# Kernel tuning notes

Hardware: AMD Instinct MI355X
Metric: run time of the kernel (lower is better)

Reference implementation:

```python
import jax, jax.numpy as jnp
import numpy as np

EPS = 1e-6
NMS_THR = 0.5
PULL_W = 1.0
PUSH_W = 1.0


def bbox_overlaps(a, b):
    # a: [M,4], b: [N,4] in (x1,y1,x2,y2) -> IoU [M,N]
    area_a = (a[:, 2] - a[:, 0]) * (a[:, 3] - a[:, 1])
    area_b = (b[:, 2] - b[:, 0]) * (b[:, 3] - b[:, 1])
    lt = jnp.maximum(a[:, None, :2], b[None, :, :2])
    rb = jnp.minimum(a[:, None, 2:], b[None, :, 2:])
    wh = jnp.clip(rb - lt, 0.0)
    inter = wh[..., 0] * wh[..., 1]
    return inter / (area_a[:, None] + area_b[None, :] - inter + EPS)


def _single_nms_loss(gti, gt_box, proposals):
    # gti: [N] int, gt_box: [G,4], proposals: [N,5]
    N = proposals.shape[0]
    G = gt_box.shape[0]
    boxes = proposals[:, :4]
    scores = proposals[:, 4]
    # push_select=True: first arg of proposal-proposal IoU is detached
    iou = bbox_overlaps(jax.lax.stop_gradient(boxes), boxes)      # [N,N]
    gpi = bbox_overlaps(gt_box, boxes)                            # [G,N]
    gpi_per = gpi[gti, jnp.arange(N)]                             # gt_proposal_iou[gt_inds[s], s]
    sg_scores = jax.lax.stop_gradient(scores)

    pos = gti >= 0
    n_pos = jnp.sum(pos)
    zero = jnp.zeros((), proposals.dtype)
    rec0 = jnp.full((G,), -1, jnp.int32)   # max_score_box_rec: gt -> box idx

    def step(carry, _):
        active, rec, pull_sum, push_sum, pull_cnt, push_cnt = carry
        any_act = jnp.any(active)
        i = jnp.argmax(jnp.where(active, scores, -jnp.inf))
        i_gt = gti[i]
        rem = active.at[i].set(False)
        has_rem = jnp.any(rem)
        body_valid = any_act & has_rem  # torch breaks before adding losses if idx empty

        # ----- pull -----
        seen = rec[i_gt] >= 0
        max_idx = jnp.maximum(rec[i_gt], 0)
        max_s_iou = jnp.maximum(iou[max_idx, i], EPS)
        pull = -jnp.log(1.0 - NMS_THR + max_s_iou) * sg_scores[i]
        pull_sum = pull_sum + jnp.where(any_act & seen & has_rem, pull, 0.0)
        pull_cnt = pull_cnt + jnp.where(any_act & seen, 1.0, 0.0)  # incremented before break
        new_val = jnp.where(any_act & ~seen, i.astype(rec.dtype), rec[i_gt])
        rec = rec.at[i_gt].set(new_val)

        # ----- push -----
        overlap = rem & (iou[i] > NMS_THR)
        push_mask = overlap & (gti != i_gt)
        has_push = jnp.any(push_mask)
        seen_s = rec[gti] >= 0  # rec already contains i_gt here (matches torch order)
        q = push_mask & (~seen_s)
        cnt = jnp.sum(q.astype(scores.dtype)) + EPS
        per = -jnp.log(EPS + gpi_per) * sg_scores
        push = jnp.sum(jnp.where(q, per, 0.0)) / cnt
        push_sum = push_sum + jnp.where(body_valid & has_push, push, 0.0)
        push_cnt = push_cnt + jnp.where(body_valid & has_push, 1.0, 0.0)

        active_next = rem & (~overlap)
        return (active_next, rec, pull_sum, push_sum, pull_cnt, push_cnt), None

    init = (pos, rec0, zero, zero, zero, zero)
    (_, _, pull_sum, push_sum, pull_cnt, push_cnt), _ = jax.lax.scan(step, init, None, length=N)

    gate = (n_pos > 1).astype(proposals.dtype)  # early-return when <=1 positive
    pull = gate * pull_sum / (pull_cnt + EPS)
    push = gate * push_sum / (push_cnt + EPS)
    return push, pull


def setup_inputs() -> dict:
    key = jax.random.key(0)
    k0, k1, k2, k3, k4, k5, k6 = jax.random.split(key, 7)
    B, N, G = 8, 2048, 64
    anchor_gt_inds = jax.random.randint(k0, (B, N), 0, G)
    # valid GT boxes: centers in a 1000x1000 image, sizes in [16,128]
    cx = jax.random.uniform(k1, (B, G)) * 1000.0
    cy = jax.random.uniform(k2, (B, G)) * 1000.0
    w = 16.0 + jax.random.uniform(k3, (B, G)) * 112.0
    h = 16.0 + jax.random.uniform(k4, (B, G)) * 112.0
    gt_bboxes = jnp.stack([cx - w / 2, cy - h / 2, cx + w / 2, cy + h / 2], axis=-1).astype(jnp.float32)
    # proposals jitter around their assigned GT so pull/push branches trigger
    pb = gt_bboxes[jnp.arange(B)[:, None], anchor_gt_inds] + jax.random.normal(k5, (B, N, 4)) * 6.0
    x1 = jnp.minimum(pb[..., 0], pb[..., 2]); x2 = jnp.maximum(pb[..., 0], pb[..., 2]) + 1.0
    y1 = jnp.minimum(pb[..., 1], pb[..., 3]); y2 = jnp.maximum(pb[..., 1], pb[..., 3]) + 1.0
    scores = jax.random.uniform(k6, (B, N))
    proposal_list = jnp.stack([x1, y1, x2, y2, scores], axis=-1).astype(jnp.float32)
    return {"gt_inds": anchor_gt_inds, "anchor_gt_inds": anchor_gt_inds,
            "gt_bboxes": gt_bboxes, "proposal_list": proposal_list}


def reference(gt_inds, anchor_gt_inds, gt_bboxes, proposal_list):
    # gt_inds is overwritten by anchor_gt_inds in the original code
    push, pull = jax.vmap(_single_nms_loss)(anchor_gt_inds, gt_bboxes, proposal_list)
    return jnp.stack([jnp.mean(push) * PUSH_W, jnp.mean(pull) * PULL_W])
```

## Files before the change

kernel.cpp:

```cpp
#include <hip/hip_runtime.h>
#include <math.h>
#include <limits.h>

#define EPSF 1e-6f
#define THR 0.5f
#define PUSH_W 1.0f
#define PULL_W 1.0f

constexpr int BN = 2048;
constexpr int BG = 64;

__device__ __forceinline__ float iou_box(float4 a, float4 b) {
  float aa = (a.z - a.x) * (a.w - a.y);
  float ab = (b.z - b.x) * (b.w - b.y);
  float w = fmaxf(fminf(a.z, b.z) - fmaxf(a.x, b.x), 0.f);
  float h = fmaxf(fminf(a.w, b.w) - fmaxf(a.y, b.y), 0.f);
  float inter = w * h;
  return inter / (aa + ab - inter + EPSF);
}

__global__ __launch_bounds__(512) void k1_sort(
    const int* __restrict__ gti_all, const float* __restrict__ gtb_all,
    const float* __restrict__ prop_all,
    float4* __restrict__ boxs, float* __restrict__ pers,
    short* __restrict__ gtss, float* __restrict__ scs,
    int* __restrict__ arrive)
{
  const int b = blockIdx.x & 7;
  const int sub = blockIdx.x >> 3;
  const int tid = threadIdx.x;
  __shared__ unsigned long long key[BN];

  if (blockIdx.x == 0 && tid == 0) *arrive = 0;

  const float* P = prop_all + (size_t)b * BN * 5;
  const int* gti = gti_all + b * BN;
  const float* GB = gtb_all + b * BG * 4;

  for (int k = 0; k < 4; ++k) {
    int j = tid + k * 512;
    key[j] = ((unsigned long long)__float_as_uint(P[j * 5 + 4]) << 32) |
             (unsigned)(BN - 1 - j);
  }
  __syncthreads();

  const int r = sub * 64 + (tid >> 3);
  const int g8 = tid & 7;
  const unsigned long long myk = key[r];
  int cnt = 0;
  const ulonglong2* K2 = (const ulonglong2*)key;
#pragma unroll 8
  for (int i = 0; i < 128; ++i) {
    ulonglong2 kk = K2[g8 + 8 * i];
    cnt += (kk.x > myk) ? 1 : 0;
    cnt += (kk.y > myk) ? 1 : 0;
  }
  cnt += __shfl_down(cnt, 4, 8);
  cnt += __shfl_down(cnt, 2, 8);
  cnt += __shfl_down(cnt, 1, 8);
  if (g8 == 0) {
    const int rank = cnt;
    int idx = (BN - 1) - (int)(myk & 0xffffffffu);
    float x1 = P[idx * 5 + 0], y1 = P[idx * 5 + 1];
    float x2 = P[idx * 5 + 2], y2 = P[idx * 5 + 3];
    float s = __uint_as_float((unsigned)(myk >> 32));
    int g = gti[idx];
    float4 bx = make_float4(x1, y1, x2, y2);
    boxs[b * BN + rank] = bx;
    scs[b * BN + rank] = s;
    gtss[b * BN + rank] = (short)g;
    float pv = 0.f;
    if (g >= 0) {
      float4 gb = make_float4(GB[g * 4], GB[g * 4 + 1], GB[g * 4 + 2], GB[g * 4 + 3]);
      pv = -logf(EPSF + iou_box(gb, bx)) * s;
    }
    pers[b * BN + rank] = pv;
  }
}

__global__ __launch_bounds__(512) void k2_adj(
    const float4* __restrict__ boxs, uint2* __restrict__ adjC)
{
  const int b  = blockIdx.x & 7;
  const int rg = (blockIdx.x >> 3) & 7;
  const int cg = blockIdx.x >> 6;
  const int tid = threadIdx.x;
  const int lane = tid & 63;
  const int w = tid >> 6;
  __shared__ float4 bs[512];

  const float4* B = boxs + b * BN;
  bs[tid] = B[cg * 512 + tid];

  const float4 r0 = B[rg * 256 +   0 + lane];
  const float4 r1 = B[rg * 256 +  64 + lane];
  const float4 r2 = B[rg * 256 + 128 + lane];
  const float4 r3 = B[rg * 256 + 192 + lane];
  const float a0 = (r0.z - r0.x) * (r0.w - r0.y) + EPSF;
  const float a1 = (r1.z - r1.x) * (r1.w - r1.y) + EPSF;
  const float a2 = (r2.z - r2.x) * (r2.w - r2.y) + EPSF;
  const float a3 = (r3.z - r3.x) * (r3.w - r3.y) + EPSF;
  __syncthreads();

  const float4* C = &bs[w * 64];
  unsigned lo0 = 0, lo1 = 0, lo2 = 0, lo3 = 0;
  unsigned hi0 = 0, hi1 = 0, hi2 = 0, hi3 = 0;

#define PRED(RR, AA, BJ, AB)                                              \
  (3.0f * (fmaxf(fminf(RR.z, BJ.z) - fmaxf(RR.x, BJ.x), 0.f) *            \
           fmaxf(fminf(RR.w, BJ.w) - fmaxf(RR.y, BJ.y), 0.f)) > AA + AB)

#pragma unroll 8
  for (int jj = 0; jj < 32; ++jj) {
    float4 bj = C[jj];
    float ab = (bj.z - bj.x) * (bj.w - bj.y);
    lo0 |= PRED(r0, a0, bj, ab) ? (1u << jj) : 0u;
    lo1 |= PRED(r1, a1, bj, ab) ? (1u << jj) : 0u;
    lo2 |= PRED(r2, a2, bj, ab) ? (1u << jj) : 0u;
    lo3 |= PRED(r3, a3, bj, ab) ? (1u << jj) : 0u;
  }
#pragma unroll 8
  for (int jj = 0; jj < 32; ++jj) {
    float4 bj = C[32 + jj];
    float ab = (bj.z - bj.x) * (bj.w - bj.y);
    hi0 |= PRED(r0, a0, bj, ab) ? (1u << jj) : 0u;
    hi1 |= PRED(r1, a1, bj, ab) ? (1u << jj) : 0u;
    hi2 |= PRED(r2, a2, bj, ab) ? (1u << jj) : 0u;
    hi3 |= PRED(r3, a3, bj, ab) ? (1u << jj) : 0u;
  }
#undef PRED

  const int c = cg * 8 + w;
  uint2* CO = adjC + ((size_t)b * 32 + c) * 2048;
  CO[rg * 256 +   0 + lane] = make_uint2(lo0, hi0);
  CO[rg * 256 +  64 + lane] = make_uint2(lo1, hi1);
  CO[rg * 256 + 128 + lane] = make_uint2(lo2, hi2);
  CO[rg * 256 + 192 + lane] = make_uint2(lo3, hi3);
}

#define QR(B, K, Q) B##_##K##_##Q

#define DECL16(B) \
  uint2 QR(B,0,0), QR(B,0,1), QR(B,0,2), QR(B,0,3), \
        QR(B,1,0), QR(B,1,1), QR(B,1,2), QR(B,1,3), \
        QR(B,2,0), QR(B,2,1), QR(B,2,2), QR(B,2,3), \
        QR(B,3,0), QR(B,3,1), QR(B,3,2), QR(B,3,3);

#define LOADCH(B, K, C) \
  QR(B,K,0) = Cb[(size_t)(C) * 2048 + wbase]; \
  QR(B,K,1) = Cb[(size_t)(C) * 2048 + wbase + 64]; \
  QR(B,K,2) = Cb[(size_t)(C) * 2048 + wbase + 128]; \
  QR(B,K,3) = Cb[(size_t)(C) * 2048 + wbase + 192];

#define LOAD16(B, RR) \
  LOADCH(B, 0, (RR)*4+0) LOADCH(B, 1, (RR)*4+1) \
  LOADCH(B, 2, (RR)*4+2) LOADCH(B, 3, (RR)*4+3)

#define PICK(B, K, C)                                                          \
  {                                                                            \
    unsigned mybit = ((act >> (K)) & ~(supG >> (K))) & 1u;                     \
    unsigned long long cand = __ballot(mybit != 0u);                           \
    unsigned long long pickw = 0ull;                                           \
    while (cand) {                                                             \
      int bpos = (int)__ffsll(cand) - 1;                                       \
      pickw |= 1ull << bpos;                                                   \
      unsigned rlo = __builtin_amdgcn_readlane(QR(B,K,K).x, bpos);             \
      unsigned rhi = __builtin_amdgcn_readlane(QR(B,K,K).y, bpos);             \
      cand &= ~((((unsigned long long)rhi) << 32) | (unsigned long long)rlo);  \
      cand &= ~(1ull << bpos);                                                 \
    }                                                                          \
    if (lane == 0) {                                                           \
      pm_lds[2 * (C)] = (unsigned)pickw;                                       \
      pm_lds[2 * (C) + 1] = (unsigned)(pickw >> 32);                           \
    }                                                                          \
    if (pickw != 0ull) {                                                       \
      unsigned pwlo = (unsigned)pickw, pwhi = (unsigned)(pickw >> 32);         \
      { unsigned hit = (QR(B,K,0).x & pwlo) | (QR(B,K,0).y & pwhi); supG |= (hit ? 1u : 0u); }      \
      { unsigned hit = (QR(B,K,1).x & pwlo) | (QR(B,K,1).y & pwhi); supG |= (hit ? 2u : 0u); }      \
      { unsigned hit = (QR(B,K,2).x & pwlo) | (QR(B,K,2).y & pwhi); supG |= (hit ? 4u : 0u); }      \
      { unsigned hit = (QR(B,K,3).x & pwlo) | (QR(B,K,3).y & pwhi); supG |= (hit ? 8u : 0u); }      \
    }                                                                          \
  }

#define APPLY(B, K, C)                                                         \
  {                                                                            \
    unsigned pwlo = pm_lds[2 * (C)], pwhi = pm_lds[2 * (C) + 1];               \
    if ((pwlo | pwhi) != 0u) {                                                 \
      unsigned nbits = 0;                                                      \
      { unsigned hit = (QR(B,K,0).x & pwlo) | (QR(B,K,0).y & pwhi); nbits |= hit ? 1u : 0u; }       \
      { unsigned hit = (QR(B,K,1).x & pwlo) | (QR(B,K,1).y & pwhi); nbits |= hit ? 2u : 0u; }       \
      { unsigned hit = (QR(B,K,2).x & pwlo) | (QR(B,K,2).y & pwhi); nbits |= hit ? 4u : 0u; }       \
      { unsigned hit = (QR(B,K,3).x & pwlo) | (QR(B,K,3).y & pwhi); nbits |= hit ? 8u : 0u; }       \
      unsigned flips = nbits & ~sup;                                           \
      sup |= nbits;                                                            \
      while (flips) {                                                          \
        int fq = __ffs(flips) - 1; flips &= flips - 1;                         \
        fsc_s[wbase + fq * 64] = (unsigned char)(C);                           \
      }                                                                        \
    }                                                                          \
  }

#define ROUND(RR, CUR, NXT)                                                    \
  {                                                                            \
    if (((RR) + 1 < 8) && (wave > (RR))) { LOAD16(NXT, (RR) + 1) }             \
    if (wave == (RR)) {                                                        \
      unsigned supG = sup;                                                     \
      PICK(CUR, 0, (RR)*4 + 0)                                                 \
      PICK(CUR, 1, (RR)*4 + 1)                                                 \
      PICK(CUR, 2, (RR)*4 + 2)                                                 \
      PICK(CUR, 3, (RR)*4 + 3)                                                 \
      asm volatile("s_waitcnt lgkmcnt(0)" ::: "memory");                       \
    }                                                                          \
    __builtin_amdgcn_s_barrier();                                              \
    asm volatile("" ::: "memory");                                             \
    if (wave >= (RR)) {                                                        \
      APPLY(CUR, 0, (RR)*4 + 0)                                                \
      APPLY(CUR, 1, (RR)*4 + 1)                                                \
      APPLY(CUR, 2, (RR)*4 + 2)                                                \
      APPLY(CUR, 3, (RR)*4 + 3)                                                \
    }                                                                          \
  }

__global__ __launch_bounds__(512, 1) void k3_fused(
    const float4* __restrict__ boxs, const float* __restrict__ pers,
    const short* __restrict__ gtss, const float* __restrict__ scs,
    const uint2* __restrict__ adjC, float* __restrict__ bp,
    int* __restrict__ arrive, float* __restrict__ out, int nb)
{
  const int b = blockIdx.x;
  const int tid = threadIdx.x;
  const int lane = tid & 63;
  const int wave = tid >> 6;

  __shared__ float qs_s[BN];
  __shared__ int qc_s[BN];
  __shared__ unsigned short ev_s[BN];
  __shared__ short gts_s[BN];
  __shared__ unsigned char fsc_s[BN];
  __shared__ unsigned pm_lds[64];
  __shared__ unsigned pre_s[64];
  __shared__ int fpr_s[64];
  __shared__ unsigned hp_s[64];
  __shared__ int lastrem_s, npick_s, npos_s;
  __shared__ float redp[8][4];

  const uint2* Cb = adjC + (size_t)b * 32 * 2048;
  const int wbase = wave * 256 + lane;

  for (int k = tid; k < BN / 2; k += 512)
    ((int*)gts_s)[k] = ((const int*)(gtss + b * BN))[k];
  for (int k = tid; k < BN; k += 512) { qs_s[k] = 0.f; qc_s[k] = 0; }
  for (int k = tid; k < BN; k += 512) fsc_s[k] = 255;
  if (tid < 64) { fpr_s[tid] = INT_MAX; hp_s[tid] = 0u; }
  if (tid == 0) { lastrem_s = 0; npos_s = 0; }
  __syncthreads();

  DECL16(X)
  DECL16(Y)
  LOAD16(X, 0)

  unsigned act = 0;
  if (gts_s[wbase +   0] >= 0) act |= 1u;
  if (gts_s[wbase +  64] >= 0) act |= 2u;
  if (gts_s[wbase + 128] >= 0) act |= 4u;
  if (gts_s[wbase + 192] >= 0) act |= 8u;
  {
    int cnt = __popc(act);
    for (int o = 1; o < 64; o <<= 1) cnt += __shfl_xor(cnt, o);
    if (lane == 0) atomicAdd(&npos_s, cnt);
  }
  unsigned sup = 0;

  ROUND(0, X, Y) ROUND(1, Y, X) ROUND(2, X, Y) ROUND(3, Y, X)
  ROUND(4, X, Y) ROUND(5, Y, X) ROUND(6, X, Y) ROUND(7, Y, X)

  __syncthreads();

  if (tid < 64) {
    int v = __popc(pm_lds[tid]);
    int inc = v;
    for (int o = 1; o < 64; o <<= 1) {
      int t = __shfl_up(inc, o);
      if (lane >= o) inc += t;
    }
    pre_s[tid] = (unsigned)(inc - v);
    if (tid == 63) npick_s = inc;
  }
  __syncthreads();
  if (wave == 0) {
    unsigned wbits = pm_lds[lane];
    int e = (int)pre_s[lane];
    while (wbits) {
      int bpos = __ffs(wbits) - 1; wbits &= wbits - 1;
      int rank = lane * 32 + bpos;
      ev_s[e] = (unsigned short)rank;
      atomicMin(&fpr_s[(int)gts_s[rank]], rank);
      e++;
    }
  }
  __syncthreads();

  const int P = npick_s;
  {
    const int j0 = tid, j1 = tid + 512, j2 = tid + 1024, j3 = tid + 1536;
    const int c0 = fsc_s[j0], c1 = fsc_s[j1], c2 = fsc_s[j2], c3 = fsc_s[j3];
    uint2 v0 = make_uint2(0, 0), v1 = v0, v2 = v0, v3 = v0;
    if (c0 != 255) v0 = Cb[(size_t)c0 * 2048 + j0];
    if (c1 != 255) v1 = Cb[(size_t)c1 * 2048 + j1];
    if (c2 != 255) v2 = Cb[(size_t)c2 * 2048 + j2];
    if (c3 != 255) v3 = Cb[(size_t)c3 * 2048 + j3];

#define PROCD(J, C, V)                                                         \
  {                                                                            \
    int gj = (int)gts_s[J];                                                    \
    if ((C) != 255 && gj >= 0) {                                               \
      unsigned m0 = V.x & pm_lds[2 * (C)];                                     \
      unsigned m1 = V.y & pm_lds[2 * (C) + 1];                                 \
      int frank = m0 ? ((C) * 64 + __ffs(m0) - 1)                              \
                     : ((C) * 64 + 32 + __ffs(m1) - 1);                        \
      if (frank != (J)) {                                                      \
        int e = (int)pre_s[frank >> 5] +                                       \
                __popc(pm_lds[frank >> 5] & ((1u << (frank & 31)) - 1u));      \
        if (e == P - 1) lastrem_s = 1;                                         \
        int gt = (int)gts_s[frank];                                            \
        if (gj != gt) {                                                        \
          atomicOr(&hp_s[e >> 5], 1u << (e & 31));                             \
          if (fpr_s[gj] > frank) {                                             \
            atomicAdd(&qs_s[e], pers[b * BN + (J)]);                           \
            atomicAdd(&qc_s[e], 1);                                            \
          }                                                                    \
        }                                                                      \
      }                                                                        \
    }                                                                          \
  }

    PROCD(j0, c0, v0)
    PROCD(j1, c1, v1)
    PROCD(j2, c2, v2)
    PROCD(j3, c3, v3)
#undef PROCD
  }
  __syncthreads();

  const int lastrem = lastrem_s;
  const int npos = npos_s;
  float pull_l = 0.f, pcl = 0.f, push_l = 0.f, pshl = 0.f;
  for (int t = tid; t < P; t += 512) {
    int r = (int)ev_s[t];
    int g = (int)gts_s[r];
    int fp = fpr_s[g];
    bool seen = (fp < r);
    bool hr = (t < P - 1) || (lastrem != 0);
    if (seen) {
      pcl += 1.f;
      if (hr) {
        float4 bA = boxs[b * BN + fp];
        float4 bB = boxs[b * BN + r];
        float io = iou_box(bA, bB);
        pull_l += -logf(1.f - THR + fmaxf(io, EPSF)) * scs[b * BN + r];
      }
    }
    if (hr && ((hp_s[t >> 5] >> (t & 31)) & 1u)) {
      pshl += 1.f;
      push_l += qs_s[t] / ((float)qc_s[t] + EPSF);
    }
  }
  for (int o = 1; o < 64; o <<= 1) {
    pull_l += __shfl_xor(pull_l, o);
    pcl    += __shfl_xor(pcl, o);
    push_l += __shfl_xor(push_l, o);
    pshl   += __shfl_xor(pshl, o);
  }
  if (lane == 0) { redp[wave][0] = pull_l; redp[wave][1] = pcl; redp[wave][2] = push_l; redp[wave][3] = pshl; }
  __syncthreads();
  if (tid == 0) {
    float Ps = 0.f, Pc = 0.f, Ss = 0.f, Sc = 0.f;
    for (int w = 0; w < 8; ++w) { Ps += redp[w][0]; Pc += redp[w][1]; Ss += redp[w][2]; Sc += redp[w][3]; }
    float gate = (npos > 1) ? 1.f : 0.f;
    bp[b * 2 + 0] = gate * Ss / (Sc + EPSF);
    bp[b * 2 + 1] = gate * Ps / (Pc + EPSF);
    __threadfence();
    int old = atomicAdd(arrive, 1);
    if (old == nb - 1) {
      __threadfence();
      float ps = 0.f, pl = 0.f;
      for (int i = 0; i < nb; ++i) { ps += bp[2 * i]; pl += bp[2 * i + 1]; }
      float inv = 1.f / (float)nb;
      out[0] = ps * inv * PUSH_W;
      out[1] = pl * inv * PULL_W;
      *arrive = 0;
    }
  }
}

constexpr int NT = 256;
constexpr int PT = BN / NT;
constexpr int NW = NT / 64;

__global__ void nms_finalize_kernel(const float* __restrict__ bp, float* __restrict__ out, int nb) {
  if (threadIdx.x == 0 && blockIdx.x == 0) {
    float ps = 0.f, pl = 0.f;
    for (int b = 0; b < nb; ++b) { ps += bp[2 * b]; pl += bp[2 * b + 1]; }
    float inv = 1.f / (float)nb;
    out[0] = ps * inv * PUSH_W;
    out[1] = pl * inv * PULL_W;
  }
}

__global__ __launch_bounds__(NT) void nms_loss_kernel(
    const int* __restrict__ gti_all, const float* __restrict__ gtb_all,
    const float* __restrict__ prop_all, float* __restrict__ out_bp)
{
  const int b = blockIdx.x;
  const int tid = threadIdx.x;
  const int lane = tid & 63;
  const int wave = tid >> 6;

  __shared__ float4 box[BN];
  __shared__ float sc[BN];
  __shared__ float per[BN];
  __shared__ int gts[BN];
  __shared__ unsigned char act[BN];
  __shared__ int rec[BG];
  __shared__ float rs[NW];
  __shared__ int ri[NW];
  __shared__ int rrem[NW];
  __shared__ int rqc[NW];
  __shared__ float rqs[NW];
  __shared__ int rany[NW];
  __shared__ int sh_nact;
  __shared__ int sh_ig;
  __shared__ float4 sh_ibox;

  const int* gti = gti_all + b * BN;
  const float* GB = gtb_all + b * BG * 4;
  const float* P = prop_all + (size_t)b * BN * 5;

  int local_pos = 0;
  for (int k = 0; k < PT; ++k) {
    int j = tid + k * NT;
    float x1 = P[j * 5 + 0], y1 = P[j * 5 + 1];
    float x2 = P[j * 5 + 2], y2 = P[j * 5 + 3];
    float s = P[j * 5 + 4];
    box[j] = make_float4(x1, y1, x2, y2);
    sc[j] = s;
    int g = gti[j];
    gts[j] = g;
    unsigned char a = (g >= 0) ? 1 : 0;
    act[j] = a;
    local_pos += a;
    float pv = 0.f;
    if (g >= 0) {
      float4 gb = make_float4(GB[g * 4], GB[g * 4 + 1], GB[g * 4 + 2], GB[g * 4 + 3]);
      float i2 = iou_box(gb, make_float4(x1, y1, x2, y2));
      pv = -logf(EPSF + i2) * s;
    }
    per[j] = pv;
  }
  if (tid < BG) rec[tid] = -1;
  for (int off = 32; off; off >>= 1) local_pos += __shfl_down(local_pos, off);
  if (lane == 0) rrem[wave] = local_pos;
  __syncthreads();
  int n_pos = 0;
  if (tid == 0) {
    for (int w = 0; w < NW; ++w) n_pos += rrem[w];
    sh_nact = n_pos;
  }
  float pull_sum = 0.f, push_sum = 0.f, pull_cnt = 0.f, push_cnt = 0.f;
  int t0_hasrem = 0;
  __syncthreads();

  while (true) {
    int nact = sh_nact;
    if (nact <= 0) break;
    float bs = -INFINITY;
    int bi = BN;
    for (int k = 0; k < PT; ++k) {
      int j = tid + k * NT;
      if (act[j]) {
        float s = sc[j];
        if (s > bs || (s == bs && j < bi)) { bs = s; bi = j; }
      }
    }
    for (int off = 32; off; off >>= 1) {
      float os = __shfl_down(bs, off);
      int oi = __shfl_down(bi, off);
      if (os > bs || (os == bs && oi < bi)) { bs = os; bi = oi; }
    }
    if (lane == 0) { rs[wave] = bs; ri[wave] = bi; }
    __syncthreads();
    if (tid == 0) {
      float cs = rs[0]; int ci = ri[0];
      for (int w = 1; w < NW; ++w)
        if (rs[w] > cs || (rs[w] == cs && ri[w] < ci)) { cs = rs[w]; ci = ri[w]; }
      int i = ci;
      int ig = gts[i];
      act[i] = 0;
      t0_hasrem = (nact - 1 > 0);
      int r = rec[ig];
      if (r >= 0) {
        pull_cnt += 1.f;
        if (t0_hasrem) {
          float i2 = iou_box(box[r], box[i]);
          float m = fmaxf(i2, EPSF);
          pull_sum += -logf(1.f - THR + m) * sc[i];
        }
      } else {
        rec[ig] = i;
      }
      sh_ig = ig; sh_ibox = box[i];
    }
    __syncthreads();
    float4 ib = sh_ibox;
    int igx = sh_ig;
    int removed = 0, qcc = 0, anyp = 0;
    float qss = 0.f;
    for (int k = 0; k < PT; ++k) {
      int j = tid + k * NT;
      if (act[j]) {
        float i2 = iou_box(ib, box[j]);
        if (i2 > THR) {
          act[j] = 0;
          removed++;
          int gj = gts[j];
          if (gj != igx) {
            anyp = 1;
            if (rec[gj] < 0) { qcc++; qss += per[j]; }
          }
        }
      }
    }
    for (int off = 32; off; off >>= 1) {
      removed += __shfl_down(removed, off);
      qcc += __shfl_down(qcc, off);
      qss += __shfl_down(qss, off);
      anyp |= __shfl_down(anyp, off);
    }
    if (lane == 0) { rrem[wave] = removed; rqc[wave] = qcc; rqs[wave] = qss; rany[wave] = anyp; }
    __syncthreads();
    if (tid == 0) {
      int rm = 0, qct = 0, ap = 0; float qst = 0.f;
      for (int w = 0; w < NW; ++w) { rm += rrem[w]; qct += rqc[w]; qst += rqs[w]; ap |= rany[w]; }
      sh_nact = nact - 1 - rm;
      if (t0_hasrem && ap) {
        push_sum += qst / ((float)qct + EPSF);
        push_cnt += 1.f;
      }
    }
    __syncthreads();
  }

  if (tid == 0) {
    float gate = (n_pos > 1) ? 1.f : 0.f;
    out_bp[b * 2 + 0] = gate * push_sum / (push_cnt + EPSF);
    out_bp[b * 2 + 1] = gate * pull_sum / (pull_cnt + EPSF);
  }
}

extern "C" void kernel_launch(void* const* d_in, const int* in_sizes, int n_in,
                              void* d_out, int out_size, void* d_ws, size_t ws_size,
                              hipStream_t stream) {
  const int* gti = (const int*)d_in[1];
  const float* gtb = (const float*)d_in[2];
  const float* props = (const float*)d_in[3];
  float* out = (float*)d_out;
  const int nb = in_sizes[1] / BN;

  const size_t off_adj  = 0;
  const size_t off_box  = off_adj  + (size_t)nb * BN * 64 * 4;
  const size_t off_per  = off_box  + (size_t)nb * BN * 16;
  const size_t off_sc   = off_per  + (size_t)nb * BN * 4;
  const size_t off_gts  = off_sc   + (size_t)nb * BN * 4;
  const size_t off_bp   = off_gts  + (size_t)nb * BN * 2;
  const size_t off_arr  = off_bp   + (size_t)nb * 2 * 4;
  const size_t needed   = off_arr + 64;

  if (ws_size >= needed && nb == 8) {
    char* ws = (char*)d_ws;
    uint2* adjC = (uint2*)(ws + off_adj);
    float4* boxs = (float4*)(ws + off_box);
    float* pers = (float*)(ws + off_per);
    float* scs = (float*)(ws + off_sc);
    short* gtss = (short*)(ws + off_gts);
    float* bp = (float*)(ws + off_bp);
    int* arrive = (int*)(ws + off_arr);

    k1_sort<<<nb * 32, 512, 0, stream>>>(gti, gtb, props, boxs, pers, gtss, scs, arrive);
    k2_adj<<<nb * 32, 512, 0, stream>>>(boxs, adjC);
    k3_fused<<<nb, 512, 0, stream>>>(boxs, pers, gtss, scs, adjC, bp, arrive, out, nb);
  } else {
    float* bp = (float*)d_ws;
    nms_loss_kernel<<<nb, NT, 0, stream>>>(gti, gtb, props, bp);
    nms_finalize_kernel<<<1, 64, 0, stream>>>(bp, out, nb);
  }
}
```

Measured before the change: 50.94 us.

## Exploit IoU symmetry in adjacency build via upper-triangle tiles and bit transpose

The adjacency kernel now computes only upper-triangular 256x256 tiles, 36 per batch instead of 64 tiles' worth of work. It writes the mirrored lower tiles by transposing each 64x64 bit block with wave shuffles. This roughly halves the IoU predicate work, but adds shuffle-based transposes and extra stores, and the grid grows to 36 smaller blocks per batch. Separately, k3 issues its first adjacency loads and the gt-active checks from global memory before the shared-memory init barrier, so that load latency overlaps the initialization.

Result: slower. 53.30 us (+4.6%).

```diff
diff --git a/kernel.cpp b/kernel.cpp
--- a/kernel.cpp
+++ b/kernel.cpp
@@ -17,6 +17,24 @@
   float h = fmaxf(fminf(a.w, b.w) - fmaxf(a.y, b.y), 0.f);
   float inter = w * h;
   return inter / (aa + ab - inter + EPSF);
+}
+
+__device__ __forceinline__ unsigned long long bittr64(unsigned long long row, int lane) {
+  const unsigned long long M0 = 0x00000000FFFFFFFFull;
+  const unsigned long long M1 = 0x0000FFFF0000FFFFull;
+  const unsigned long long M2 = 0x00FF00FF00FF00FFull;
+  const unsigned long long M3 = 0x0F0F0F0F0F0F0F0Full;
+  const unsigned long long M4 = 0x3333333333333333ull;
+  const unsigned long long M5 = 0x5555555555555555ull;
+#define TSTEP(m, j)                                                      \
+  {                                                                      \
+    unsigned long long t = __shfl_xor(row, j);                           \
+    if ((lane & (j)) == 0) row = (row & (m)) | ((t & (m)) << (j));       \
+    else                   row = (row & ~(m)) | ((t >> (j)) & (m));      \
+  }
+  TSTEP(M0, 32) TSTEP(M1, 16) TSTEP(M2, 8) TSTEP(M3, 4) TSTEP(M4, 2) TSTEP(M5, 1)
+#undef TSTEP
+  return row;
 }
 
 __global__ __launch_bounds__(512) void k1_sort(
@@ -81,30 +99,32 @@
 __global__ __launch_bounds__(512) void k2_adj(
     const float4* __restrict__ boxs, uint2* __restrict__ adjC)
 {
-  const int b  = blockIdx.x & 7;
-  const int rg = (blockIdx.x >> 3) & 7;
-  const int cg = blockIdx.x >> 6;
+  const int b = blockIdx.x & 7;
+  const int t = blockIdx.x >> 3;
+  int rg = 0, acc = 0;
+  while (acc + (8 - rg) <= t) { acc += 8 - rg; rg++; }
+  const int ct = rg + (t - acc);
+
   const int tid = threadIdx.x;
   const int lane = tid & 63;
   const int w = tid >> 6;
-  __shared__ float4 bs[512];
+  const int rh = w >> 2;
+  const int cc = w & 3;
+  __shared__ float4 bs[256];
 
   const float4* B = boxs + b * BN;
-  bs[tid] = B[cg * 512 + tid];
-
-  const float4 r0 = B[rg * 256 +   0 + lane];
-  const float4 r1 = B[rg * 256 +  64 + lane];
-  const float4 r2 = B[rg * 256 + 128 + lane];
-  const float4 r3 = B[rg * 256 + 192 + lane];
+  if (tid < 256) bs[tid] = B[ct * 256 + tid];
+
+  const int row0 = rg * 256 + rh * 128 + lane;
+  const int row1 = row0 + 64;
+  const float4 r0 = B[row0];
+  const float4 r1 = B[row1];
   const float a0 = (r0.z - r0.x) * (r0.w - r0.y) + EPSF;
   const float a1 = (r1.z - r1.x) * (r1.w - r1.y) + EPSF;
-  const float a2 = (r2.z - r2.x) * (r2.w - r2.y) + EPSF;
-  const float a3 = (r3.z - r3.x) * (r3.w - r3.y) + EPSF;
-  __syncthreads();
-
-  const float4* C = &bs[w * 64];
-  unsigned lo0 = 0, lo1 = 0, lo2 = 0, lo3 = 0;
-  unsigned hi0 = 0, hi1 = 0, hi2 = 0, hi3 = 0;
+  __syncthreads();
+
+  const float4* C = &bs[cc * 64];
+  unsigned lo0 = 0, hi0 = 0, lo1 = 0, hi1 = 0;
 
 #define PRED(RR, AA, BJ, AB)                                              \
   (3.0f * (fmaxf(fminf(RR.z, BJ.z) - fmaxf(RR.x, BJ.x), 0.f) *            \
@@ -116,8 +136,6 @@
     float ab = (bj.z - bj.x) * (bj.w - bj.y);
     lo0 |= PRED(r0, a0, bj, ab) ? (1u << jj) : 0u;
     lo1 |= PRED(r1, a1, bj, ab) ? (1u << jj) : 0u;
-    lo2 |= PRED(r2, a2, bj, ab) ? (1u << jj) : 0u;
-    lo3 |= PRED(r3, a3, bj, ab) ? (1u << jj) : 0u;
   }
 #pragma unroll 8
   for (int jj = 0; jj < 32; ++jj) {
@@ -125,17 +143,24 @@
     float ab = (bj.z - bj.x) * (bj.w - bj.y);
     hi0 |= PRED(r0, a0, bj, ab) ? (1u << jj) : 0u;
     hi1 |= PRED(r1, a1, bj, ab) ? (1u << jj) : 0u;
-    hi2 |= PRED(r2, a2, bj, ab) ? (1u << jj) : 0u;
-    hi3 |= PRED(r3, a3, bj, ab) ? (1u << jj) : 0u;
   }
 #undef PRED
 
-  const int c = cg * 8 + w;
-  uint2* CO = adjC + ((size_t)b * 32 + c) * 2048;
-  CO[rg * 256 +   0 + lane] = make_uint2(lo0, hi0);
-  CO[rg * 256 +  64 + lane] = make_uint2(lo1, hi1);
-  CO[rg * 256 + 128 + lane] = make_uint2(lo2, hi2);
-  CO[rg * 256 + 192 + lane] = make_uint2(lo3, hi3);
+  uint2* CO = adjC + ((size_t)b * 32 + ct * 4 + cc) * 2048;
+  CO[row0] = make_uint2(lo0, hi0);
+  CO[row1] = make_uint2(lo1, hi1);
+
+  if (ct != rg) {
+    unsigned long long t0 = ((unsigned long long)hi0 << 32) | (unsigned long long)lo0;
+    unsigned long long t1 = ((unsigned long long)hi1 << 32) | (unsigned long long)lo1;
+    t0 = bittr64(t0, lane);
+    t1 = bittr64(t1, lane);
+    const int mrow = ct * 256 + cc * 64 + lane;
+    uint2* M0 = adjC + ((size_t)b * 32 + rg * 4 + rh * 2) * 2048;
+    uint2* M1 = adjC + ((size_t)b * 32 + rg * 4 + rh * 2 + 1) * 2048;
+    M0[mrow] = make_uint2((unsigned)t0, (unsigned)(t0 >> 32));
+    M1[mrow] = make_uint2((unsigned)t1, (unsigned)(t1 >> 32));
+  }
 }
 
 #define QR(B, K, Q) B##_##K##_##Q
@@ -247,6 +272,15 @@
   const uint2* Cb = adjC + (size_t)b * 32 * 2048;
   const int wbase = wave * 256 + lane;
 
+  DECL16(X)
+  DECL16(Y)
+  LOAD16(X, 0)
+  unsigned act = 0;
+  if (gtss[b * BN + wbase +   0] >= 0) act |= 1u;
+  if (gtss[b * BN + wbase +  64] >= 0) act |= 2u;
+  if (gtss[b * BN + wbase + 128] >= 0) act |= 4u;
+  if (gtss[b * BN + wbase + 192] >= 0) act |= 8u;
+
   for (int k = tid; k < BN / 2; k += 512)
     ((int*)gts_s)[k] = ((const int*)(gtss + b * BN))[k];
   for (int k = tid; k < BN; k += 512) { qs_s[k] = 0.f; qc_s[k] = 0; }
@@ -255,15 +289,6 @@
   if (tid == 0) { lastrem_s = 0; npos_s = 0; }
   __syncthreads();
 
-  DECL16(X)
-  DECL16(Y)
-  LOAD16(X, 0)
-
-  unsigned act = 0;
-  if (gts_s[wbase +   0] >= 0) act |= 1u;
-  if (gts_s[wbase +  64] >= 0) act |= 2u;
-  if (gts_s[wbase + 128] >= 0) act |= 4u;
-  if (gts_s[wbase + 192] >= 0) act |= 8u;
   {
     int cnt = __popc(act);
     for (int o = 1; o < 64; o <<= 1) cnt += __shfl_xor(cnt, o);
@@ -586,7 +611,7 @@
     int* arrive = (int*)(ws + off_arr);
 
     k1_sort<<<nb * 32, 512, 0, stream>>>(gti, gtb, props, boxs, pers, gtss, scs, arrive);
-    k2_adj<<<nb * 32, 512, 0, stream>>>(boxs, adjC);
+    k2_adj<<<nb * 36, 512, 0, stream>>>(boxs, adjC);
     k3_fused<<<nb, 512, 0, stream>>>(boxs, pers, gtss, scs, adjC, bp, arrive, out, nb);
   } else {
     float* bp = (float*)d_ws;
```
